# Performance work log

Hardware: AMD Instinct MI355X
Metric: run time of the kernel (lower is better)

The kernel has to match this reference:

```python
import jax, jax.numpy as jnp
import numpy as np

B = 65536      # batch
CTX = 512      # raw context features
POS = 2        # lat/lon
IN = CTX + POS # 514, RNNCell 0 input dim
HID = 128      # hidden_dim
OBS = 8        # observed trajectory length
PRED = 12      # pred_len


def setup_inputs() -> dict:
    key = jax.random.key(0)
    ks = jax.random.split(key, 16)
    inp = {
        "raw_ctx": jax.random.normal(ks[0], (B, CTX), jnp.float32),
        "obs_traj": jax.random.normal(ks[1], (OBS, B, POS), jnp.float32),
    }
    # RNNCell params: h' = tanh(x @ Wih.T + bih + h @ Whh.T + bhh)
    dims = [IN, HID, HID]  # input dims of the 3 stacked cells
    i = 2
    for l, d in enumerate(dims):
        inp[f"Wih{l}"] = jax.random.normal(ks[i], (HID, d), jnp.float32) / np.sqrt(d).astype(np.float32); i += 1
        inp[f"Whh{l}"] = jax.random.normal(ks[i], (HID, HID), jnp.float32) / np.sqrt(HID).astype(np.float32); i += 1
        inp[f"bih{l}"] = jnp.zeros((HID,), jnp.float32)
        inp[f"bhh{l}"] = jnp.zeros((HID,), jnp.float32)
    # fc: xavier-ish small init, zero bias (matches _init_weights)
    inp["fcW"] = jax.random.normal(ks[i], (POS, HID), jnp.float32) * 0.05
    inp["fcb"] = jnp.zeros((POS,), jnp.float32)
    return inp


def reference(raw_ctx, obs_traj,
              Wih0, Whh0, bih0, bhh0,
              Wih1, Whh1, bih1, bhh1,
              Wih2, Whh2, bih2, bhh2,
              fcW, fcb):
    sg = jax.lax.stop_gradient
    hid = Wih0.shape[0]
    Bn = raw_ctx.shape[0]

    def cell(x, h_prev, Wih, Whh, bih, bhh):
        # torch code detaches the previous hidden state: h_list[j].detach()
        return jnp.tanh(x @ Wih.T + bih + sg(h_prev) @ Whh.T + bhh)

    def step(carry, _):
        (h0, h1, h2), pos = carry
        inp = jnp.concatenate([raw_ctx, pos], axis=-1)  # [B, 514]
        h0 = cell(inp, h0, Wih0, Whh0, bih0, bhh0)
        h1 = cell(h0, h1, Wih1, Whh1, bih1, bhh1)
        h2 = cell(h1, h2, Wih2, Whh2, bih2, bhh2)
        out = h2 @ fcW.T + fcb                          # [B, 2]
        # feed_forward=True: cur_pos = output.detach()
        return ((h0, h1, h2), sg(out)), out

    z = jnp.zeros((Bn, hid), raw_ctx.dtype)
    init = ((z, z, z), obs_traj[-1])  # initial cur_pos = obs_traj[-1] (not detached)
    _, preds = jax.lax.scan(step, init, None, length=PRED)
    return preds  # [pred_len, B, 2]
```

## Files before the change

kernel.cpp:

```cpp
#include <hip/hip_runtime.h>
#include <cstdint>
#include <cstddef>


#define BATCH    65536
#define CTXF     512
#define INF      514
#define HID      128
#define PREDL    12
#define OBSL     8
#define BM       64
#define NTHREADS 512

typedef __attribute__((ext_vector_type(8))) short s16x8;
typedef __attribute__((ext_vector_type(4))) float f32x4;

#define MFMA16(a, b, c) __builtin_amdgcn_mfma_f32_16x16x32_bf16((a), (b), (c), 0, 0, 0)

__device__ __forceinline__ unsigned int cvt_pk(float a, float b) {
    unsigned int r;
    asm("v_cvt_pk_bf16_f32 %0, %1, %2" : "=v"(r) : "v"(a), "v"(b));
    return r;
}
__device__ __forceinline__ float ubf(unsigned int bits) { return __uint_as_float(bits); }
__device__ __forceinline__ float bf2f(short h) {
    return __uint_as_float(((unsigned int)(unsigned short)h) << 16);
}

union Frag { unsigned int u[4]; s16x8 v; };

__device__ __forceinline__ void split8(const float* x, s16x8& hi, s16x8& lo) {
    Frag H, L;
#pragma unroll
    for (int i = 0; i < 4; ++i) {
        unsigned int hp = cvt_pk(x[2 * i], x[2 * i + 1]);
        float r0 = x[2 * i]     - ubf(hp << 16);
        float r1 = x[2 * i + 1] - ubf(hp & 0xffff0000u);
        H.u[i] = hp;
        L.u[i] = cvt_pk(r0, r1);
    }
    hi = H.v; lo = L.v;
}

__device__ __forceinline__ float fast_tanh(float x) {
    float e = __expf(x + x);
    float r = __builtin_amdgcn_rcpf(e + 1.0f);
    return fmaf(-2.0f, r, 1.0f);
}

__device__ __forceinline__ void load_w(const float* __restrict__ W, int ldw,
                                       int n0, int lane, s16x8* hi, s16x8* lo) {
    const float* base = W + (size_t)(n0 + (lane & 15)) * ldw + ((lane >> 4) * 8);
#pragma unroll
    for (int kt = 0; kt < 4; ++kt) {
        float x[8];
        *(float4*)(x)     = *(const float4*)(base + kt * 32);
        *(float4*)(x + 4) = *(const float4*)(base + kt * 32 + 4);
        split8(x, hi[kt], lo[kt]);
    }
}

__device__ __forceinline__ void mat_pass(f32x4* acc,
                                         const s16x8* whi, const s16x8* wlo,
                                         const unsigned short* __restrict__ phi,
                                         const unsigned short* __restrict__ plo,
                                         int lane) {
    const int i15 = lane & 15;
    const int sx  = (i15 & 7) << 3;
    const int kb0 = (lane >> 4) * 8;
#pragma unroll
    for (int kt = 0; kt < 4; ++kt) {
        const int kbs = (kt * 32 + kb0) ^ sx;
#pragma unroll
        for (int g = 0; g < 4; ++g) {
            const int idx = (g * 16 + i15) * HID + kbs;
            s16x8 bh = *reinterpret_cast<const s16x8*>(&phi[idx]);
            s16x8 bl = *reinterpret_cast<const s16x8*>(&plo[idx]);
            acc[g] = MFMA16(whi[kt], bh, acc[g]);
            acc[g] = MFMA16(whi[kt], bl, acc[g]);
            acc[g] = MFMA16(wlo[kt], bh, acc[g]);
        }
    }
}

__global__ void __launch_bounds__(NTHREADS, 2)
rnn_head_kernel(const float* __restrict__ raw_ctx,
                const float* __restrict__ obs_traj,
                const float* __restrict__ Wih0, const float* __restrict__ Whh0,
                const float* __restrict__ bih0, const float* __restrict__ bhh0,
                const float* __restrict__ Wih1, const float* __restrict__ Whh1,
                const float* __restrict__ bih1, const float* __restrict__ bhh1,
                const float* __restrict__ Wih2, const float* __restrict__ Whh2,
                const float* __restrict__ bih2, const float* __restrict__ bhh2,
                const float* __restrict__ fcW,  const float* __restrict__ fcb,
                float* __restrict__ out)
{
    __shared__ __align__(16) unsigned short h_hi[3][BM * HID];
    __shared__ __align__(16) unsigned short h_lo[3][BM * HID];
    __shared__ float pbuf[BM][2];
    __shared__ float fcw_s[2][HID];
    __shared__ __align__(16) float ctx_s[BM][132];

    const int tid  = threadIdx.x;
    const int lane = tid & 63;
    const int wid  = __builtin_amdgcn_readfirstlane(tid >> 6);
    const int n0   = wid * 16;
    const int row0 = blockIdx.x * BM;
    const int i15  = lane & 15;
    const int h4   = lane >> 4;
    const int nb   = n0 + h4 * 4;
    const int sx   = (i15 & 7) << 3;
    const int nbs  = nb ^ sx;

    f32x4 b0, b1, b2, wp0, wp1;
#pragma unroll
    for (int r = 0; r < 4; ++r) {
        b0[r]  = bih0[nb + r] + bhh0[nb + r];
        b1[r]  = bih1[nb + r] + bhh1[nb + r];
        b2[r]  = bih2[nb + r] + bhh2[nb + r];
        wp0[r] = Wih0[(size_t)(nb + r) * INF + 512];
        wp1[r] = Wih0[(size_t)(nb + r) * INF + 513];
    }
    const float fcb0 = fcb[0], fcb1 = fcb[1];

    for (int i = tid; i < 3 * BM * HID / 2; i += NTHREADS) {
        ((unsigned int*)h_hi)[i] = 0u;
        ((unsigned int*)h_lo)[i] = 0u;
    }
    if (tid < BM) {
        const float2 pv = *reinterpret_cast<const float2*>(
            &obs_traj[((size_t)(OBSL - 1) * BATCH + row0 + tid) * 2]);
        pbuf[tid][0] = pv.x; pbuf[tid][1] = pv.y;
    }
    if (tid < 2 * HID) fcw_s[tid >> 7][tid & 127] = fcW[tid];

    f32x4 ctxc[4];
#pragma unroll
    for (int g = 0; g < 4; ++g) ctxc[g] = b0;

#pragma unroll 1
    for (int kc = 0; kc < CTXF; kc += 128) {
        s16x8 cah[4], cal[4];
        {
            const float* base = Wih0 + (size_t)(n0 + i15) * INF + kc + h4 * 8;
#pragma unroll
            for (int kt = 0; kt < 4; ++kt) {
                float x[8];
                *(float4*)(x)     = *(const float4*)(base + kt * 32);
                *(float4*)(x + 4) = *(const float4*)(base + kt * 32 + 4);
                split8(x, cah[kt], cal[kt]);
            }
        }
        __syncthreads();
        {
            const int rr = tid >> 3, seg = (tid & 7) * 16;
            const float* src = raw_ctx + (size_t)(row0 + rr) * CTXF + kc + seg;
            float4 v0 = ((const float4*)src)[0], v1 = ((const float4*)src)[1];
            float4 v2 = ((const float4*)src)[2], v3 = ((const float4*)src)[3];
            float* dst = &ctx_s[rr][seg];
            ((float4*)dst)[0] = v0; ((float4*)dst)[1] = v1;
            ((float4*)dst)[2] = v2; ((float4*)dst)[3] = v3;
        }
        __syncthreads();
#pragma unroll
        for (int kt = 0; kt < 4; ++kt) {
#pragma unroll
            for (int g = 0; g < 4; ++g) {
                const int m = g * 16 + i15;
                const float* xp = &ctx_s[m][kt * 32 + h4 * 8];
                float x[8];
                *(float4*)(x)     = *(const float4*)(xp);
                *(float4*)(x + 4) = *(const float4*)(xp + 4);
                s16x8 bh, bl;
                split8(x, bh, bl);
                ctxc[g] = MFMA16(cah[kt], bh, ctxc[g]);
                ctxc[g] = MFMA16(cah[kt], bl, ctxc[g]);
                ctxc[g] = MFMA16(cal[kt], bh, ctxc[g]);
            }
        }
    }

    s16x8 whh0h[4], whh0l[4], wih1h[4], wih1l[4], whh1h[4], whh1l[4];
    s16x8 wih2h[4], wih2l[4], whh2h[4], whh2l[4];
    load_w(Whh0, HID, n0, lane, whh0h, whh0l);
    load_w(Wih1, HID, n0, lane, wih1h, wih1l);
    load_w(Whh1, HID, n0, lane, whh1h, whh1l);
    load_w(Wih2, HID, n0, lane, wih2h, wih2l);
    load_w(Whh2, HID, n0, lane, whh2h, whh2l);

    __syncthreads();

#pragma unroll 1
    for (int s = 0; s < PREDL; ++s) {
        f32x4 acc[4];

#pragma unroll
        for (int g = 0; g < 4; ++g) {
            acc[g] = ctxc[g];
            const float2 p = *reinterpret_cast<const float2*>(&pbuf[g * 16 + i15][0]);
#pragma unroll
            for (int r = 0; r < 4; ++r) {
                acc[g][r] = fmaf(p.x, wp0[r], acc[g][r]);
                acc[g][r] = fmaf(p.y, wp1[r], acc[g][r]);
            }
        }
        mat_pass(acc, whh0h, whh0l, h_hi[0], h_lo[0], lane);
        __syncthreads();
#pragma unroll
        for (int g = 0; g < 4; ++g) {
            const int mi = (g * 16 + i15) * HID + nbs;
            float t0 = fast_tanh(acc[g][0]), t1 = fast_tanh(acc[g][1]);
            float t2 = fast_tanh(acc[g][2]), t3 = fast_tanh(acc[g][3]);
            unsigned int hp0 = cvt_pk(t0, t1), hp1 = cvt_pk(t2, t3);
            unsigned int lp0 = cvt_pk(t0 - ubf(hp0 << 16), t1 - ubf(hp0 & 0xffff0000u));
            unsigned int lp1 = cvt_pk(t2 - ubf(hp1 << 16), t3 - ubf(hp1 & 0xffff0000u));
            *reinterpret_cast<uint2*>(&h_hi[0][mi]) = make_uint2(hp0, hp1);
            *reinterpret_cast<uint2*>(&h_lo[0][mi]) = make_uint2(lp0, lp1);
        }
        __syncthreads();

#pragma unroll
        for (int g = 0; g < 4; ++g) {
#pragma unroll
            for (int r = 0; r < 4; ++r) acc[g][r] = b1[r];
        }
        mat_pass(acc, wih1h, wih1l, h_hi[0], h_lo[0], lane);
        mat_pass(acc, whh1h, whh1l, h_hi[1], h_lo[1], lane);
        __syncthreads();
#pragma unroll
        for (int g = 0; g < 4; ++g) {
            const int mi = (g * 16 + i15) * HID + nbs;
            float t0 = fast_tanh(acc[g][0]), t1 = fast_tanh(acc[g][1]);
            float t2 = fast_tanh(acc[g][2]), t3 = fast_tanh(acc[g][3]);
            unsigned int hp0 = cvt_pk(t0, t1), hp1 = cvt_pk(t2, t3);
            unsigned int lp0 = cvt_pk(t0 - ubf(hp0 << 16), t1 - ubf(hp0 & 0xffff0000u));
            unsigned int lp1 = cvt_pk(t2 - ubf(hp1 << 16), t3 - ubf(hp1 & 0xffff0000u));
            *reinterpret_cast<uint2*>(&h_hi[1][mi]) = make_uint2(hp0, hp1);
            *reinterpret_cast<uint2*>(&h_lo[1][mi]) = make_uint2(lp0, lp1);
        }
        __syncthreads();

#pragma unroll
        for (int g = 0; g < 4; ++g) {
#pragma unroll
            for (int r = 0; r < 4; ++r) acc[g][r] = b2[r];
        }
        mat_pass(acc, wih2h, wih2l, h_hi[1], h_lo[1], lane);
        mat_pass(acc, whh2h, whh2l, h_hi[2], h_lo[2], lane);
        __syncthreads();
#pragma unroll
        for (int g = 0; g < 4; ++g) {
            const int mi = (g * 16 + i15) * HID + nbs;
            float t0 = fast_tanh(acc[g][0]), t1 = fast_tanh(acc[g][1]);
            float t2 = fast_tanh(acc[g][2]), t3 = fast_tanh(acc[g][3]);
            unsigned int hp0 = cvt_pk(t0, t1), hp1 = cvt_pk(t2, t3);
            unsigned int lp0 = cvt_pk(t0 - ubf(hp0 << 16), t1 - ubf(hp0 & 0xffff0000u));
            unsigned int lp1 = cvt_pk(t2 - ubf(hp1 << 16), t3 - ubf(hp1 & 0xffff0000u));
            *reinterpret_cast<uint2*>(&h_hi[2][mi]) = make_uint2(hp0, hp1);
            *reinterpret_cast<uint2*>(&h_lo[2][mi]) = make_uint2(lp0, lp1);
        }
        __syncthreads();

        if (wid < 2) {
            const int m = lane, c = wid;
            const int sxf = (m & 7) << 3;
            float o = (c == 0) ? fcb0 : fcb1;
#pragma unroll
            for (int kb = 0; kb < HID; kb += 8) {
                const int idx = m * HID + (kb ^ sxf);
                s16x8 hv = *reinterpret_cast<const s16x8*>(&h_hi[2][idx]);
                s16x8 lv = *reinterpret_cast<const s16x8*>(&h_lo[2][idx]);
                float wv[8];
                *(float4*)(wv)     = *(const float4*)(&fcw_s[c][kb]);
                *(float4*)(wv + 4) = *(const float4*)(&fcw_s[c][kb + 4]);
#pragma unroll
                for (int j = 0; j < 8; ++j) {
                    float x = bf2f(hv[j]) + bf2f(lv[j]);
                    o = fmaf(x, wv[j], o);
                }
            }
            pbuf[m][c] = o;
            out[((size_t)s * BATCH + row0 + m) * 2 + c] = o;
        }
        __syncthreads();
    }
}

extern "C" void kernel_launch(void* const* d_in, const int* in_sizes, int n_in,
                              void* d_out, int out_size, void* d_ws, size_t ws_size,
                              hipStream_t stream)
{
    const float* raw_ctx  = (const float*)d_in[0];
    const float* obs_traj = (const float*)d_in[1];
    const float* Wih0 = (const float*)d_in[2];
    const float* Whh0 = (const float*)d_in[3];
    const float* bih0 = (const float*)d_in[4];
    const float* bhh0 = (const float*)d_in[5];
    const float* Wih1 = (const float*)d_in[6];
    const float* Whh1 = (const float*)d_in[7];
    const float* bih1 = (const float*)d_in[8];
    const float* bhh1 = (const float*)d_in[9];
    const float* Wih2 = (const float*)d_in[10];
    const float* Whh2 = (const float*)d_in[11];
    const float* bih2 = (const float*)d_in[12];
    const float* bhh2 = (const float*)d_in[13];
    const float* fcW  = (const float*)d_in[14];
    const float* fcb  = (const float*)d_in[15];
    float* out = (float*)d_out;

    dim3 grid(BATCH / BM);
    dim3 block(NTHREADS);
    rnn_head_kernel<<<grid, block, 0, stream>>>(
        raw_ctx, obs_traj,
        Wih0, Whh0, bih0, bhh0,
        Wih1, Whh1, bih1, bhh1,
        Wih2, Whh2, bih2, bhh2,
        fcW, fcb, out);
}
```

Baseline: 708.2 us.

## Reschedule RNN step to overlap recurrent matmuls and fuse FC head into epilogue

Each step now runs the recurrent-weight products for layers 1 and 2 (Whh1·h1, Whh2·h2) early, alongside layer 0 and layer 1, because they depend only on the previous step's state. This cuts the per-step barrier count from 7 to 4. The separate FC head pass over the stored hidden state is replaced by partial dot products in the layer-2 epilogue, reduced with cross-lane shuffles and a small shared buffer. The position feedback now comes through registers and shuffles instead of a shared pbuf. Biases move from registers to shared memory, which eases register pressure but adds LDS reads and keeps three accumulator sets live at once.

```diff
diff --git a/kernel.cpp b/kernel.cpp
--- a/kernel.cpp
+++ b/kernel.cpp
@@ -23,9 +23,6 @@
     return r;
 }
 __device__ __forceinline__ float ubf(unsigned int bits) { return __uint_as_float(bits); }
-__device__ __forceinline__ float bf2f(short h) {
-    return __uint_as_float(((unsigned int)(unsigned short)h) << 16);
-}
 
 union Frag { unsigned int u[4]; s16x8 v; };
 
@@ -97,9 +94,9 @@
 {
     __shared__ __align__(16) unsigned short h_hi[3][BM * HID];
     __shared__ __align__(16) unsigned short h_lo[3][BM * HID];
-    __shared__ float pbuf[BM][2];
-    __shared__ float fcw_s[2][HID];
     __shared__ __align__(16) float ctx_s[BM][132];
+    __shared__ __align__(16) float cst[4][HID];
+    __shared__ float2 pfc[8][BM];
 
     const int tid  = threadIdx.x;
     const int lane = tid & 63;
@@ -112,27 +109,28 @@
     const int sx   = (i15 & 7) << 3;
     const int nbs  = nb ^ sx;
 
-    f32x4 b0, b1, b2, wp0, wp1;
+    f32x4 b0, wp0, wp1;
 #pragma unroll
     for (int r = 0; r < 4; ++r) {
         b0[r]  = bih0[nb + r] + bhh0[nb + r];
-        b1[r]  = bih1[nb + r] + bhh1[nb + r];
-        b2[r]  = bih2[nb + r] + bhh2[nb + r];
         wp0[r] = Wih0[(size_t)(nb + r) * INF + 512];
         wp1[r] = Wih0[(size_t)(nb + r) * INF + 513];
     }
     const float fcb0 = fcb[0], fcb1 = fcb[1];
 
+    if (tid < HID) {
+        cst[0][tid] = bih1[tid] + bhh1[tid];
+        cst[1][tid] = bih2[tid] + bhh2[tid];
+        cst[2][tid] = fcW[tid];
+        cst[3][tid] = fcW[HID + tid];
+    }
     for (int i = tid; i < 3 * BM * HID / 2; i += NTHREADS) {
         ((unsigned int*)h_hi)[i] = 0u;
         ((unsigned int*)h_lo)[i] = 0u;
     }
-    if (tid < BM) {
-        const float2 pv = *reinterpret_cast<const float2*>(
-            &obs_traj[((size_t)(OBSL - 1) * BATCH + row0 + tid) * 2]);
-        pbuf[tid][0] = pv.x; pbuf[tid][1] = pv.y;
-    }
-    if (tid < 2 * HID) fcw_s[tid >> 7][tid & 127] = fcW[tid];
+    float2 pv = *reinterpret_cast<const float2*>(
+        &obs_traj[((size_t)(OBSL - 1) * BATCH + row0 + lane) * 2]);
+    float o0 = pv.x, o1 = pv.y;
 
     f32x4 ctxc[4];
 #pragma unroll
@@ -192,97 +190,104 @@
 
 #pragma unroll 1
     for (int s = 0; s < PREDL; ++s) {
-        f32x4 acc[4];
-
-#pragma unroll
-        for (int g = 0; g < 4; ++g) {
-            acc[g] = ctxc[g];
-            const float2 p = *reinterpret_cast<const float2*>(&pbuf[g * 16 + i15][0]);
+        f32x4 acc0[4], acc1[4], acc2[4];
+
+#pragma unroll
+        for (int g = 0; g < 4; ++g) {
+            const float pxg = __shfl(o0, g * 16 + i15);
+            const float pyg = __shfl(o1, g * 16 + i15);
+            f32x4 a = ctxc[g];
 #pragma unroll
             for (int r = 0; r < 4; ++r) {
-                acc[g][r] = fmaf(p.x, wp0[r], acc[g][r]);
-                acc[g][r] = fmaf(p.y, wp1[r], acc[g][r]);
-            }
-        }
-        mat_pass(acc, whh0h, whh0l, h_hi[0], h_lo[0], lane);
-        __syncthreads();
+                a[r] = fmaf(pxg, wp0[r], a[r]);
+                a[r] = fmaf(pyg, wp1[r], a[r]);
+            }
+            acc0[g] = a;
+            f32x4 z; z[0] = 0.f; z[1] = 0.f; z[2] = 0.f; z[3] = 0.f;
+            acc1[g] = z;
+        }
+        mat_pass(acc0, whh0h, whh0l, h_hi[0], h_lo[0], lane);
+        mat_pass(acc1, whh1h, whh1l, h_hi[1], h_lo[1], lane);
+        unsigned int pk0[4][4];
+#pragma unroll
+        for (int g = 0; g < 4; ++g) {
+            float t0 = fast_tanh(acc0[g][0]), t1 = fast_tanh(acc0[g][1]);
+            float t2 = fast_tanh(acc0[g][2]), t3 = fast_tanh(acc0[g][3]);
+            unsigned int hp0 = cvt_pk(t0, t1), hp1 = cvt_pk(t2, t3);
+            pk0[g][0] = hp0; pk0[g][1] = hp1;
+            pk0[g][2] = cvt_pk(t0 - ubf(hp0 << 16), t1 - ubf(hp0 & 0xffff0000u));
+            pk0[g][3] = cvt_pk(t2 - ubf(hp1 << 16), t3 - ubf(hp1 & 0xffff0000u));
+        }
+        __syncthreads();
+
 #pragma unroll
         for (int g = 0; g < 4; ++g) {
             const int mi = (g * 16 + i15) * HID + nbs;
-            float t0 = fast_tanh(acc[g][0]), t1 = fast_tanh(acc[g][1]);
-            float t2 = fast_tanh(acc[g][2]), t3 = fast_tanh(acc[g][3]);
+            *reinterpret_cast<uint2*>(&h_hi[0][mi]) = make_uint2(pk0[g][0], pk0[g][1]);
+            *reinterpret_cast<uint2*>(&h_lo[0][mi]) = make_uint2(pk0[g][2], pk0[g][3]);
+        }
+        __syncthreads();
+
+#pragma unroll
+        for (int g = 0; g < 4; ++g) {
+            f32x4 z; z[0] = 0.f; z[1] = 0.f; z[2] = 0.f; z[3] = 0.f;
+            acc2[g] = z;
+        }
+        mat_pass(acc1, wih1h, wih1l, h_hi[0], h_lo[0], lane);
+        mat_pass(acc2, whh2h, whh2l, h_hi[2], h_lo[2], lane);
+#pragma unroll
+        for (int g = 0; g < 4; ++g) {
+            f32x4 b = *reinterpret_cast<const f32x4*>(&cst[0][nb]);
+            float t0 = fast_tanh(acc1[g][0] + b[0]), t1 = fast_tanh(acc1[g][1] + b[1]);
+            float t2 = fast_tanh(acc1[g][2] + b[2]), t3 = fast_tanh(acc1[g][3] + b[3]);
             unsigned int hp0 = cvt_pk(t0, t1), hp1 = cvt_pk(t2, t3);
             unsigned int lp0 = cvt_pk(t0 - ubf(hp0 << 16), t1 - ubf(hp0 & 0xffff0000u));
             unsigned int lp1 = cvt_pk(t2 - ubf(hp1 << 16), t3 - ubf(hp1 & 0xffff0000u));
-            *reinterpret_cast<uint2*>(&h_hi[0][mi]) = make_uint2(hp0, hp1);
-            *reinterpret_cast<uint2*>(&h_lo[0][mi]) = make_uint2(lp0, lp1);
-        }
-        __syncthreads();
-
-#pragma unroll
-        for (int g = 0; g < 4; ++g) {
-#pragma unroll
-            for (int r = 0; r < 4; ++r) acc[g][r] = b1[r];
-        }
-        mat_pass(acc, wih1h, wih1l, h_hi[0], h_lo[0], lane);
-        mat_pass(acc, whh1h, whh1l, h_hi[1], h_lo[1], lane);
-        __syncthreads();
-#pragma unroll
-        for (int g = 0; g < 4; ++g) {
             const int mi = (g * 16 + i15) * HID + nbs;
-            float t0 = fast_tanh(acc[g][0]), t1 = fast_tanh(acc[g][1]);
-            float t2 = fast_tanh(acc[g][2]), t3 = fast_tanh(acc[g][3]);
-            unsigned int hp0 = cvt_pk(t0, t1), hp1 = cvt_pk(t2, t3);
-            unsigned int lp0 = cvt_pk(t0 - ubf(hp0 << 16), t1 - ubf(hp0 & 0xffff0000u));
-            unsigned int lp1 = cvt_pk(t2 - ubf(hp1 << 16), t3 - ubf(hp1 & 0xffff0000u));
             *reinterpret_cast<uint2*>(&h_hi[1][mi]) = make_uint2(hp0, hp1);
             *reinterpret_cast<uint2*>(&h_lo[1][mi]) = make_uint2(lp0, lp1);
         }
         __syncthreads();
 
-#pragma unroll
-        for (int g = 0; g < 4; ++g) {
-#pragma unroll
-            for (int r = 0; r < 4; ++r) acc[g][r] = b2[r];
-        }
-        mat_pass(acc, wih2h, wih2l, h_hi[1], h_lo[1], lane);
-        mat_pass(acc, whh2h, whh2l, h_hi[2], h_lo[2], lane);
-        __syncthreads();
-#pragma unroll
-        for (int g = 0; g < 4; ++g) {
+        mat_pass(acc2, wih2h, wih2l, h_hi[1], h_lo[1], lane);
+#pragma unroll
+        for (int g = 0; g < 4; ++g) {
+            f32x4 b  = *reinterpret_cast<const f32x4*>(&cst[1][nb]);
+            f32x4 f0 = *reinterpret_cast<const f32x4*>(&cst[2][nb]);
+            f32x4 f1 = *reinterpret_cast<const f32x4*>(&cst[3][nb]);
+            float t[4];
+            float p0 = 0.f, p1 = 0.f;
+#pragma unroll
+            for (int r = 0; r < 4; ++r) {
+                t[r] = fast_tanh(acc2[g][r] + b[r]);
+                p0 = fmaf(t[r], f0[r], p0);
+                p1 = fmaf(t[r], f1[r], p1);
+            }
+            unsigned int hp0 = cvt_pk(t[0], t[1]), hp1 = cvt_pk(t[2], t[3]);
+            unsigned int lp0 = cvt_pk(t[0] - ubf(hp0 << 16), t[1] - ubf(hp0 & 0xffff0000u));
+            unsigned int lp1 = cvt_pk(t[2] - ubf(hp1 << 16), t[3] - ubf(hp1 & 0xffff0000u));
             const int mi = (g * 16 + i15) * HID + nbs;
-            float t0 = fast_tanh(acc[g][0]), t1 = fast_tanh(acc[g][1]);
-            float t2 = fast_tanh(acc[g][2]), t3 = fast_tanh(acc[g][3]);
-            unsigned int hp0 = cvt_pk(t0, t1), hp1 = cvt_pk(t2, t3);
-            unsigned int lp0 = cvt_pk(t0 - ubf(hp0 << 16), t1 - ubf(hp0 & 0xffff0000u));
-            unsigned int lp1 = cvt_pk(t2 - ubf(hp1 << 16), t3 - ubf(hp1 & 0xffff0000u));
             *reinterpret_cast<uint2*>(&h_hi[2][mi]) = make_uint2(hp0, hp1);
             *reinterpret_cast<uint2*>(&h_lo[2][mi]) = make_uint2(lp0, lp1);
-        }
-        __syncthreads();
-
-        if (wid < 2) {
-            const int m = lane, c = wid;
-            const int sxf = (m & 7) << 3;
-            float o = (c == 0) ? fcb0 : fcb1;
-#pragma unroll
-            for (int kb = 0; kb < HID; kb += 8) {
-                const int idx = m * HID + (kb ^ sxf);
-                s16x8 hv = *reinterpret_cast<const s16x8*>(&h_hi[2][idx]);
-                s16x8 lv = *reinterpret_cast<const s16x8*>(&h_lo[2][idx]);
-                float wv[8];
-                *(float4*)(wv)     = *(const float4*)(&fcw_s[c][kb]);
-                *(float4*)(wv + 4) = *(const float4*)(&fcw_s[c][kb + 4]);
-#pragma unroll
-                for (int j = 0; j < 8; ++j) {
-                    float x = bf2f(hv[j]) + bf2f(lv[j]);
-                    o = fmaf(x, wv[j], o);
-                }
-            }
-            pbuf[m][c] = o;
-            out[((size_t)s * BATCH + row0 + m) * 2 + c] = o;
-        }
-        __syncthreads();
+            p0 += __shfl_xor(p0, 16); p0 += __shfl_xor(p0, 32);
+            p1 += __shfl_xor(p1, 16); p1 += __shfl_xor(p1, 32);
+            if (h4 == 0) pfc[wid][g * 16 + i15] = make_float2(p0, p1);
+        }
+        __syncthreads();
+
+        {
+            float s0 = fcb0, s1 = fcb1;
+#pragma unroll
+            for (int w = 0; w < 8; ++w) {
+                float2 q = pfc[w][lane];
+                s0 += q.x; s1 += q.y;
+            }
+            o0 = s0; o1 = s1;
+            if (wid == 0) {
+                *reinterpret_cast<float2*>(&out[((size_t)s * BATCH + row0 + lane) * 2]) =
+                    make_float2(s0, s1);
+            }
+        }
     }
 }
 
```

Result: faster. 659.0 us (-6.9%).
